# Optimization experiments

Hardware: AMD Instinct MI355X
Metric: run time of the kernel (lower is better)

The kernel has to match this reference:

```python
import jax, jax.numpy as jnp
import numpy as np

N_NODES = 50000
N_EDGES = 1200000
F_IN = 128
F_EDGE = 32
H = 78


def _p(key, shape, fan_in):
    return jax.random.normal(key, shape, dtype=jnp.float32) / np.sqrt(fan_in)


def setup_inputs() -> dict:
    key = jax.random.key(0)
    ks = jax.random.split(key, 20)
    x = jax.random.normal(ks[0], (N_NODES, F_IN), dtype=jnp.float32)
    edge_index = jax.random.randint(ks[1], (2, N_EDGES), 0, N_NODES, dtype=jnp.int32)
    edge_attr = jax.random.normal(ks[2], (N_EDGES, F_EDGE), dtype=jnp.float32)
    return {
        "x": x, "edge_index": edge_index, "edge_attr": edge_attr,
        # GATConv layer 1
        "W1": _p(ks[3], (F_IN, H), F_IN), "as1": _p(ks[4], (H,), H), "ad1": _p(ks[5], (H,), H),
        "b1": jnp.zeros((H,), jnp.float32),
        # GATConv layer 2
        "W2": _p(ks[6], (H, H), H), "as2": _p(ks[7], (H,), H), "ad2": _p(ks[8], (H,), H),
        "b2": jnp.zeros((H,), jnp.float32),
        # edge MLP
        "Wm1": _p(ks[9], (F_EDGE, H), F_EDGE), "bm1": jnp.zeros((H,), jnp.float32),
        "Wm2": _p(ks[10], (H, H), H), "bm2": jnp.zeros((H,), jnp.float32),
        # final edge head
        "Wf": _p(ks[11], (3 * H, 1), 3 * H), "bf": jnp.zeros((1,), jnp.float32),
    }


def _gat_conv(x, W, a_src, a_dst, bias, src, dst, n_nodes):
    """PyG GATConv, heads=1, negative_slope=0.2, self-loops already in src/dst."""
    h = x @ W                                   # [N, H]
    alpha_s = h @ a_src                         # [N]
    alpha_d = h @ a_dst                         # [N]
    e = jax.nn.leaky_relu(alpha_s[src] + alpha_d[dst], negative_slope=0.2)  # [E']
    # softmax over incoming edges per destination node
    m = jax.ops.segment_max(e, dst, num_segments=n_nodes)
    e = jnp.exp(e - m[dst])
    s = jax.ops.segment_sum(e, dst, num_segments=n_nodes)
    alpha = e / (s[dst] + 1e-16)                # [E']
    out = jax.ops.segment_sum(alpha[:, None] * h[src], dst, num_segments=n_nodes)
    return out + bias


def reference(x, edge_index, edge_attr, W1, as1, ad1, b1, W2, as2, ad2, b2,
              Wm1, bm1, Wm2, bm2, Wf, bf):
    n_nodes = x.shape[0]
    loop = jnp.arange(n_nodes, dtype=edge_index.dtype)
    src = jnp.concatenate([edge_index[0], loop])  # add self-loops (PyG default)
    dst = jnp.concatenate([edge_index[1], loop])

    h = _gat_conv(x, W1, as1, ad1, b1, src, dst, n_nodes)
    h = jax.nn.relu(h)  # dropout is identity in eval mode
    h = _gat_conv(h, W2, as2, ad2, b2, src, dst, n_nodes)

    ef = jax.nn.relu(edge_attr @ Wm1 + bm1) @ Wm2 + bm2            # [E, H]
    emb = jnp.concatenate([h[edge_index[0]], h[edge_index[1]], ef], axis=1)  # [E, 3H]
    return jnp.squeeze(emb @ Wf + bf, axis=-1)                     # [E]
```

## Files before the change

kernel.cpp:

```cpp
#include <hip/hip_runtime.h>
#include <math.h>

#define NN 50000
#define NE 1200000
#define FIN 128
#define FE 32
#define H 78
#define HP 80
#define ETOT (NE + NN)

#define NPB 64
#define NBUCK ((NN + NPB - 1) / NPB)
#define BCAP 2560

#define EB 3200
#define NBE ((ETOT + EB - 1) / EB)
#define GHN (NBUCK * NBE)
#define GS_NB ((GHN + 1023) / 1024)

typedef __attribute__((ext_vector_type(8))) short bf16x8;
typedef __attribute__((ext_vector_type(4))) float f32x4;

__device__ __forceinline__ unsigned short f2bf(float f) {
  unsigned u = __float_as_uint(f);
  return (unsigned short)((u + 0x7FFFu + ((u >> 16) & 1u)) >> 16);
}
__device__ __forceinline__ float bf2f(unsigned short b) {
  return __uint_as_float((unsigned)b << 16);
}

union Frag { uint4 q; bf16x8 v; unsigned short u[8]; };

__device__ __forceinline__ void wperm_one(const float* __restrict__ W, int K, int idx,
                                          uint4* __restrict__ out) {
  int lane = idx & 63;
  int fid = idx >> 6;
  int split = fid & 1;
  int sg = fid >> 1;
  int step = sg / 5, g = sg % 5;
  int kg = lane >> 4, l15 = lane & 15;
  int col = g * 16 + l15;
  Frag f;
#pragma unroll
  for (int e = 0; e < 8; ++e) {
    int k = step * 32 + kg * 8 + e;
    float v = (k < K && col < H) ? W[(size_t)k * H + col] : 0.f;
    unsigned short h = f2bf(v);
    if (split) h = f2bf(v - bf2f(h));
    f.u[e] = h;
  }
  out[idx] = f.q;
}

__global__ void prep_all(const float* __restrict__ W1, const float* __restrict__ W2,
                         const float* __restrict__ Wm2, const float* __restrict__ bm2,
                         const float* __restrict__ Wf, const float* __restrict__ bf,
                         uint4* __restrict__ wperm1, uint4* __restrict__ wperm2,
                         float* __restrict__ wpc) {
  int b = blockIdx.x, t = threadIdx.x;
  if (b < 10) {
    wperm_one(W1, FIN, b * 256 + t, wperm1);
  } else if (b < 18) {
    int idx = (b - 10) * 256 + t;
    if (idx < 30 * 64) wperm_one(W2, H, idx, wperm2);
  } else {
    int k = t;
    if (k < H) {
      float s = 0.f;
      for (int j = 0; j < H; ++j) s += Wm2[k * H + j] * Wf[2 * H + j];
      wpc[k] = s;
    } else if (k == H) {
      float s = 0.f;
      for (int j = 0; j < H; ++j) s += bm2[j] * Wf[2 * H + j];
      wpc[H] = s + bf[0];
    }
  }
}

template<int STEPS, int LDA>
__global__ __launch_bounds__(256)
void gemm_mfma(const float* __restrict__ A, const uint4* __restrict__ wperm,
               const float* __restrict__ as, const float* __restrict__ ad,
               unsigned* __restrict__ hb, float* __restrict__ asv,
               float* __restrict__ adv) {
  int lane = threadIdx.x & 63;
  int gw = blockIdx.x * 4 + (threadIdx.x >> 6);
  int n0w = gw * 16;
  if (n0w >= NN) return;
  int l15 = lane & 15, kg = lane >> 4;
  f32x4 acc[5];
#pragma unroll
  for (int g = 0; g < 5; ++g) acc[g] = (f32x4){0.f, 0.f, 0.f, 0.f};

#pragma unroll
  for (int step = 0; step < STEPS; ++step) {
    int k0 = step * 32 + kg * 8;
    bf16x8 ah, al;
    if (k0 < LDA) {
      int row = n0w + l15;
      if (row >= NN) row = NN - 1;
      const float* ar = A + (size_t)row * LDA + k0;
      float4 f0 = *reinterpret_cast<const float4*>(ar);
      float4 f1 = *reinterpret_cast<const float4*>(ar + 4);
      float fv[8] = {f0.x, f0.y, f0.z, f0.w, f1.x, f1.y, f1.z, f1.w};
#pragma unroll
      for (int e = 0; e < 8; ++e) {
        unsigned short h = f2bf(fv[e]);
        ah[e] = (short)h;
        al[e] = (short)f2bf(fv[e] - bf2f(h));
      }
    } else {
#pragma unroll
      for (int e = 0; e < 8; ++e) { ah[e] = 0; al[e] = 0; }
    }
#pragma unroll
    for (int g = 0; g < 5; ++g) {
      Frag wh, wl;
      wh.q = wperm[((size_t)(step * 5 + g) * 2 + 0) * 64 + lane];
      wl.q = wperm[((size_t)(step * 5 + g) * 2 + 1) * 64 + lane];
      acc[g] = __builtin_amdgcn_mfma_f32_16x16x32_bf16(ah, wh.v, acc[g], 0, 0, 0);
      acc[g] = __builtin_amdgcn_mfma_f32_16x16x32_bf16(al, wh.v, acc[g], 0, 0, 0);
      acc[g] = __builtin_amdgcn_mfma_f32_16x16x32_bf16(ah, wl.v, acc[g], 0, 0, 0);
    }
  }

  float asl[5], adl[5];
#pragma unroll
  for (int g = 0; g < 5; ++g) {
    int col = g * 16 + l15;
    asl[g] = (col < H) ? as[col] : 0.f;
    adl[g] = (col < H) ? ad[col] : 0.f;
  }

#pragma unroll
  for (int r = 0; r < 4; ++r) {
    int node = n0w + kg * 4 + r;
#pragma unroll
    for (int g = 0; g < 5; ++g) {
      float c = acc[g][r];
      float cn = __shfl_xor(c, 1);
      if (!(l15 & 1) && node < NN)
        hb[(size_t)node * (HP / 2) + g * 8 + (l15 >> 1)] =
            (unsigned)f2bf(c) | ((unsigned)f2bf(cn) << 16);
    }
    float sa = 0.f, sd = 0.f;
#pragma unroll
    for (int g = 0; g < 5; ++g) {
      sa = fmaf(acc[g][r], asl[g], sa);
      sd = fmaf(acc[g][r], adl[g], sd);
    }
#pragma unroll
    for (int mask = 1; mask < 16; mask <<= 1) {
      sa += __shfl_xor(sa, mask);
      sd += __shfl_xor(sd, mask);
    }
    if (l15 == 0 && node < NN) { asv[node] = sa; adv[node] = sd; }
  }
}

__global__ __launch_bounds__(256)
void bin_hist(const int* __restrict__ ei, int* __restrict__ gh) {
  __shared__ int hist[NBUCK];
  int b = blockIdx.x, t = threadIdx.x;
  for (int k = t; k < NBUCK; k += 256) hist[k] = 0;
  __syncthreads();
  int e0 = b * EB;
  int e1 = min(e0 + EB, ETOT);
  for (int i = e0 + t; i < e1; i += 256) {
    int dst = (i < NE) ? ei[NE + i] : (i - NE);
    atomicAdd(&hist[dst >> 6], 1);
  }
  __syncthreads();
  for (int k = t; k < NBUCK; k += 256) gh[(size_t)k * NBE + b] = hist[k];
}

__global__ void scan1g(const int* __restrict__ gh, int* __restrict__ gsum) {
  __shared__ int sh[256];
  int b = blockIdx.x, t = threadIdx.x;
  int i0 = b * 1024 + t * 4;
  int s = 0;
#pragma unroll
  for (int k = 0; k < 4; ++k) {
    int i = i0 + k;
    if (i < GHN) s += gh[i];
  }
  sh[t] = s;
  __syncthreads();
  for (int off = 128; off > 0; off >>= 1) {
    if (t < off) sh[t] += sh[t + off];
    __syncthreads();
  }
  if (t == 0) gsum[b] = sh[0];
}

__global__ void scan2g(const int* __restrict__ gsum, int* __restrict__ gboff) {
  __shared__ int sh[512];
  int t = threadIdx.x;
  sh[t] = (t < GS_NB) ? gsum[t] : 0;
  __syncthreads();
  for (int off = 1; off < 512; off <<= 1) {
    int v = (t >= off) ? sh[t - off] : 0;
    __syncthreads();
    sh[t] += v;
    __syncthreads();
  }
  if (t < GS_NB) gboff[t] = (t == 0) ? 0 : sh[t - 1];
}

__global__ void scan3g(const int* __restrict__ gh, const int* __restrict__ gboff,
                       int* __restrict__ goff) {
  __shared__ int sh[256];
  int b = blockIdx.x, t = threadIdx.x;
  int i0 = b * 1024 + t * 4;
  int v[4];
  int s = 0;
#pragma unroll
  for (int k = 0; k < 4; ++k) {
    int i = i0 + k;
    v[k] = (i < GHN) ? gh[i] : 0;
    s += v[k];
  }
  sh[t] = s;
  __syncthreads();
  for (int off = 1; off < 256; off <<= 1) {
    int u = (t >= off) ? sh[t - off] : 0;
    __syncthreads();
    sh[t] += u;
    __syncthreads();
  }
  int run = gboff[b] + ((t == 0) ? 0 : sh[t - 1]);
#pragma unroll
  for (int k = 0; k < 4; ++k) {
    int i = i0 + k;
    if (i < GHN) { goff[i] = run; run += v[k]; }
  }
}

__global__ __launch_bounds__(256)
void bin_place(const int* __restrict__ ei, const int* __restrict__ goff,
               unsigned long long* __restrict__ tmp) {
  __shared__ int cursor[NBUCK];
  int b = blockIdx.x, t = threadIdx.x;
  for (int k = t; k < NBUCK; k += 256) cursor[k] = goff[(size_t)k * NBE + b];
  __syncthreads();
  int e0 = b * EB;
  int e1 = min(e0 + EB, ETOT);
  for (int i = e0 + t; i < e1; i += 256) {
    int src, dst;
    if (i < NE) { src = ei[i]; dst = ei[NE + i]; }
    else { src = dst = i - NE; }
    int pos = atomicAdd(&cursor[dst >> 6], 1);
    tmp[pos] = ((unsigned long long)(unsigned)dst << 32) | (unsigned)src;
  }
}

__global__ __launch_bounds__(256)
void bucket_build(const unsigned long long* __restrict__ tmp,
                  const int* __restrict__ goff,
                  int* __restrict__ rowptr, int* __restrict__ srcs) {
  __shared__ int hist[NPB];
  __shared__ int offs[NPB];
  __shared__ int curs[NPB];
  __shared__ int srcs_l[BCAP];
  int b = blockIdx.x, t = threadIdx.x;
  int base = goff[(size_t)b * NBE];
  int next = (b + 1 < NBUCK) ? goff[(size_t)(b + 1) * NBE] : ETOT;
  int cnt = next - base;
  int n0 = b * NPB;
  if (t < NPB) hist[t] = 0;
  __syncthreads();
  for (int p = t; p < cnt; p += 256) {
    int dst = (int)(tmp[base + p] >> 32);
    atomicAdd(&hist[dst - n0], 1);
  }
  __syncthreads();
  if (t == 0) {
    int run = 0;
    for (int j = 0; j < NPB; ++j) { offs[j] = run; run += hist[j]; }
  }
  __syncthreads();
  if (t < NPB) {
    curs[t] = offs[t];
    int n = n0 + t;
    if (n < NN) rowptr[n] = base + offs[t];
  }
  if (b == NBUCK - 1 && t == 0) rowptr[NN] = ETOT;
  __syncthreads();
  for (int p = t; p < cnt; p += 256) {
    unsigned long long e = tmp[base + p];
    int dst = (int)(e >> 32);
    int src = (int)(e & 0xffffffffULL);
    int lp = atomicAdd(&curs[dst - n0], 1);
    if (lp < BCAP) srcs_l[lp] = src;
    else srcs[base + lp] = src;
  }
  __syncthreads();
  int m = cnt < BCAP ? cnt : BCAP;
  for (int p = t; p < m; p += 256) srcs[base + p] = srcs_l[p];
}

template<int RELU, int FINAL>
__global__ __launch_bounds__(256)
void gat_fused(const int* __restrict__ rowptr, const int* __restrict__ srcs,
               const float* __restrict__ asv, const float* __restrict__ adv,
               const unsigned* __restrict__ hb, const float* __restrict__ bias,
               const float* __restrict__ Wf, float* __restrict__ outp,
               float* __restrict__ uu, float* __restrict__ vv) {
  int n = (blockIdx.x * 256 + threadIdx.x) >> 6;
  int lane = threadIdx.x & 63;
  if (n >= NN) return;
  int r0 = rowptr[n], r1 = rowptr[n + 1];
  int deg = r1 - r0;
  float advn = adv[n];

  int s0 = 0;
  float e0 = -INFINITY;
  if (lane < deg) {
    s0 = srcs[r0 + lane];
    float e = asv[s0] + advn;
    e0 = e > 0.f ? e : 0.2f * e;
  }
  float m = e0;
#pragma unroll
  for (int off = 1; off < 64; off <<= 1) m = fmaxf(m, __shfl_xor(m, off));
  float ssum = (lane < deg) ? __expf(e0 - m) : 0.f;
#pragma unroll
  for (int off = 1; off < 64; off <<= 1) ssum += __shfl_xor(ssum, off);
  for (int c = r0 + 64; c < r1; c += 64) {
    int p = c + lane;
    float e = -INFINITY;
    if (p < r1) {
      float t = asv[srcs[p]] + advn;
      e = t > 0.f ? t : 0.2f * t;
    }
    float cm = e;
#pragma unroll
    for (int off = 1; off < 64; off <<= 1) cm = fmaxf(cm, __shfl_xor(cm, off));
    float c2 = (p < r1) ? __expf(e - cm) : 0.f;
#pragma unroll
    for (int off = 1; off < 64; off <<= 1) c2 += __shfl_xor(c2, off);
    float mn = fmaxf(m, cm);
    ssum = ssum * __expf(m - mn) + c2 * __expf(cm - mn);
    m = mn;
  }
  float inv = 1.f / (ssum + 1e-16f);
  float alpha0 = (lane < deg) ? __expf(e0 - m) * inv : 0.f;

  int g3 = lane / 20;
  int lp = lane - g3 * 20;
  float4 acc = {0.f, 0.f, 0.f, 0.f};
  int nch = deg < 64 ? deg : 64;
  for (int base = 0; base < nch; base += 3) {
    int p = base + g3;
    bool act = (g3 < 3) && (p < nch);
    int idx = p < 63 ? p : 63;
    float al = __shfl(alpha0, idx);
    int s = __shfl(s0, idx);
    if (act) {
      uint2 w01 = *reinterpret_cast<const uint2*>(hb + (size_t)s * (HP / 2) + lp * 2);
      acc.x = fmaf(al, bf2f((unsigned short)(w01.x & 0xffff)), acc.x);
      acc.y = fmaf(al, bf2f((unsigned short)(w01.x >> 16)), acc.y);
      acc.z = fmaf(al, bf2f((unsigned short)(w01.y & 0xffff)), acc.z);
      acc.w = fmaf(al, bf2f((unsigned short)(w01.y >> 16)), acc.w);
    }
  }
  for (int c = r0 + 64; c < r1; c += 64) {
    int p = c + lane;
    float al = 0.f;
    int s = 0;
    if (p < r1) {
      s = srcs[p];
      float t = asv[s] + advn;
      t = t > 0.f ? t : 0.2f * t;
      al = __expf(t - m) * inv;
    }
    int cnt = min(r1 - c, 64);
    for (int base = 0; base < cnt; base += 3) {
      int p2 = base + g3;
      bool act = (g3 < 3) && (p2 < cnt);
      int idx = p2 < 63 ? p2 : 63;
      float alq = __shfl(al, idx);
      int sq = __shfl(s, idx);
      if (act) {
        uint2 w01 = *reinterpret_cast<const uint2*>(hb + (size_t)sq * (HP / 2) + lp * 2);
        acc.x = fmaf(alq, bf2f((unsigned short)(w01.x & 0xffff)), acc.x);
        acc.y = fmaf(alq, bf2f((unsigned short)(w01.x >> 16)), acc.y);
        acc.z = fmaf(alq, bf2f((unsigned short)(w01.y & 0xffff)), acc.z);
        acc.w = fmaf(alq, bf2f((unsigned short)(w01.y >> 16)), acc.w);
      }
    }
  }

  float4 a1, a2;
  a1.x = __shfl(acc.x, lane + 20); a1.y = __shfl(acc.y, lane + 20);
  a1.z = __shfl(acc.z, lane + 20); a1.w = __shfl(acc.w, lane + 20);
  a2.x = __shfl(acc.x, lane + 40); a2.y = __shfl(acc.y, lane + 40);
  a2.z = __shfl(acc.z, lane + 40); a2.w = __shfl(acc.w, lane + 40);

  if (FINAL) {
    float su = 0.f, sv = 0.f;
    if (lane < 20) {
      int c0 = lane * 4;
      float o0 = acc.x + a1.x + a2.x + ((c0 + 0 < H) ? bias[c0 + 0] : 0.f);
      float o1 = acc.y + a1.y + a2.y + ((c0 + 1 < H) ? bias[c0 + 1] : 0.f);
      float o2 = acc.z + a1.z + a2.z + ((c0 + 2 < H) ? bias[c0 + 2] : 0.f);
      float o3 = acc.w + a1.w + a2.w + ((c0 + 3 < H) ? bias[c0 + 3] : 0.f);
      float wu0 = (c0 + 0 < H) ? Wf[c0 + 0] : 0.f;
      float wu1 = (c0 + 1 < H) ? Wf[c0 + 1] : 0.f;
      float wu2 = (c0 + 2 < H) ? Wf[c0 + 2] : 0.f;
      float wu3 = (c0 + 3 < H) ? Wf[c0 + 3] : 0.f;
      float wv0 = (c0 + 0 < H) ? Wf[H + c0 + 0] : 0.f;
      float wv1 = (c0 + 1 < H) ? Wf[H + c0 + 1] : 0.f;
      float wv2 = (c0 + 2 < H) ? Wf[H + c0 + 2] : 0.f;
      float wv3 = (c0 + 3 < H) ? Wf[H + c0 + 3] : 0.f;
      su = o0 * wu0 + o1 * wu1 + o2 * wu2 + o3 * wu3;
      sv = o0 * wv0 + o1 * wv1 + o2 * wv2 + o3 * wv3;
    }
#pragma unroll
    for (int off = 1; off < 64; off <<= 1) {
      su += __shfl_xor(su, off);
      sv += __shfl_xor(sv, off);
    }
    if (lane == 0) { uu[n] = su; vv[n] = sv; }
  } else {
    if (lane < 20) {
      int c0 = lane * 4;
      float4 o;
      o.x = acc.x + a1.x + a2.x + ((c0 + 0 < H) ? bias[c0 + 0] : 0.f);
      o.y = acc.y + a1.y + a2.y + ((c0 + 1 < H) ? bias[c0 + 1] : 0.f);
      o.z = acc.z + a1.z + a2.z + ((c0 + 2 < H) ? bias[c0 + 2] : 0.f);
      o.w = acc.w + a1.w + a2.w + ((c0 + 3 < H) ? bias[c0 + 3] : 0.f);
      if (RELU) {
        o.x = fmaxf(o.x, 0.f); o.y = fmaxf(o.y, 0.f);
        o.z = fmaxf(o.z, 0.f); o.w = fmaxf(o.w, 0.f);
      }
      *reinterpret_cast<float4*>(outp + (size_t)n * HP + c0) = o;
    }
  }
}

#define FE_WAVES 18750
__global__ __launch_bounds__(256)
void final_edge_mfma(const int* __restrict__ ei, const float* __restrict__ ea,
                     const float* __restrict__ Wm1, const float* __restrict__ bm1,
                     const float* __restrict__ wpc, const float* __restrict__ u,
                     const float* __restrict__ v, float* __restrict__ out) {
  int lane = threadIdx.x & 63;
  long gw = (long)blockIdx.x * 4 + (threadIdx.x >> 6);
  if (gw >= FE_WAVES) return;
  int l15 = lane & 15;
  int kg = lane >> 4;
  bf16x8 bfrag[5];
  float bm1c[5], wpcc[5];
#pragma unroll
  for (int g = 0; g < 5; ++g) {
    int col = g * 16 + l15;
    bool valid = col < H;
    bm1c[g] = valid ? bm1[col] : 0.f;
    wpcc[g] = valid ? wpc[col] : 0.f;
#pragma unroll
    for (int e = 0; e < 8; ++e) {
      int kk = kg * 8 + e;
      bfrag[g][e] = valid ? (short)f2bf(Wm1[kk * H + col]) : (short)0;
    }
  }
  float basec = wpc[H];
  int e0 = (int)(gw * 64);
#pragma unroll
  for (int t = 0; t < 4; ++t) {
    int ebase = e0 + t * 16;
    const float* ar = ea + (size_t)(ebase + l15) * FE + kg * 8;
    float4 f0 = *reinterpret_cast<const float4*>(ar);
    float4 f1 = *reinterpret_cast<const float4*>(ar + 4);
    bf16x8 afrag;
    afrag[0] = (short)f2bf(f0.x); afrag[1] = (short)f2bf(f0.y);
    afrag[2] = (short)f2bf(f0.z); afrag[3] = (short)f2bf(f0.w);
    afrag[4] = (short)f2bf(f1.x); afrag[5] = (short)f2bf(f1.y);
    afrag[6] = (short)f2bf(f1.z); afrag[7] = (short)f2bf(f1.w);
    float es0 = 0.f, es1 = 0.f, es2 = 0.f, es3 = 0.f;
#pragma unroll
    for (int g = 0; g < 5; ++g) {
      f32x4 c = {0.f, 0.f, 0.f, 0.f};
      c = __builtin_amdgcn_mfma_f32_16x16x32_bf16(afrag, bfrag[g], c, 0, 0, 0);
      es0 = fmaf(fmaxf(c[0] + bm1c[g], 0.f), wpcc[g], es0);
      es1 = fmaf(fmaxf(c[1] + bm1c[g], 0.f), wpcc[g], es1);
      es2 = fmaf(fmaxf(c[2] + bm1c[g], 0.f), wpcc[g], es2);
      es3 = fmaf(fmaxf(c[3] + bm1c[g], 0.f), wpcc[g], es3);
    }
#pragma unroll
    for (int m = 1; m < 16; m <<= 1) {
      es0 += __shfl_xor(es0, m);
      es1 += __shfl_xor(es1, m);
      es2 += __shfl_xor(es2, m);
      es3 += __shfl_xor(es3, m);
    }
    if (l15 < 4) {
      float es = (l15 == 0) ? es0 : (l15 == 1) ? es1 : (l15 == 2) ? es2 : es3;
      int e = ebase + kg * 4 + l15;
      int s = ei[e], d = ei[NE + e];
      out[e] = es + u[s] + v[d] + basec;
    }
  }
}

extern "C" void kernel_launch(void* const* d_in, const int* in_sizes, int n_in,
                              void* d_out, int out_size, void* d_ws, size_t ws_size,
                              hipStream_t stream) {
  const float* x   = (const float*)d_in[0];
  const int*   ei  = (const int*)d_in[1];
  const float* ea  = (const float*)d_in[2];
  const float* W1  = (const float*)d_in[3];
  const float* as1 = (const float*)d_in[4];
  const float* ad1 = (const float*)d_in[5];
  const float* b1  = (const float*)d_in[6];
  const float* W2  = (const float*)d_in[7];
  const float* as2 = (const float*)d_in[8];
  const float* ad2 = (const float*)d_in[9];
  const float* b2  = (const float*)d_in[10];
  const float* Wm1 = (const float*)d_in[11];
  const float* bm1 = (const float*)d_in[12];
  const float* Wm2 = (const float*)d_in[13];
  const float* bm2 = (const float*)d_in[14];
  const float* Wf  = (const float*)d_in[15];
  const float* bf  = (const float*)d_in[16];
  float* out = (float*)d_out;

  float* w = (float*)d_ws;
  float* bufB = w; w += (size_t)NN * HP;
  unsigned* hb = (unsigned*)w; w += (size_t)NN * (HP / 2);
  uint4* wperm1 = (uint4*)w; w += 4 * 40 * 64;
  uint4* wperm2 = (uint4*)w; w += 4 * 30 * 64;
  float* asv  = w; w += NN;
  float* adv  = w; w += NN;
  float* uu   = w; w += NN;
  float* vv   = w; w += NN;
  float* wpc  = w; w += HP;
  unsigned long long* tmp = (unsigned long long*)w; w += 2 * (size_t)ETOT;
  int* rowptr = (int*)w; w += NN + 1;
  int* srcs   = (int*)w; w += ETOT;
  int* gh     = (int*)w; w += GHN;
  int* goff   = (int*)w; w += GHN;
  int* gsum   = (int*)w; w += GS_NB;
  int* gboff  = (int*)w; w += GS_NB;

  const int B = 256;
  dim3 gG((NN + 63) / 64);
  dim3 gW((NN * 64 + B - 1) / B);
  dim3 gFE((FE_WAVES + 3) / 4);

  prep_all<<<19, B, 0, stream>>>(W1, W2, Wm2, bm2, Wf, bf, wperm1, wperm2, wpc);

  bin_hist<<<NBE, B, 0, stream>>>(ei, gh);
  scan1g<<<GS_NB, B, 0, stream>>>(gh, gsum);
  scan2g<<<1, 512, 0, stream>>>(gsum, gboff);
  scan3g<<<GS_NB, B, 0, stream>>>(gh, gboff, goff);
  bin_place<<<NBE, B, 0, stream>>>(ei, goff, tmp);
  bucket_build<<<NBUCK, B, 0, stream>>>(tmp, goff, rowptr, srcs);

  gemm_mfma<4, FIN><<<gG, B, 0, stream>>>(x, wperm1, as1, ad1, hb, asv, adv);
  gat_fused<1, 0><<<gW, B, 0, stream>>>(rowptr, srcs, asv, adv, hb, b1, Wf,
                                        bufB, uu, vv);

  gemm_mfma<3, HP><<<gG, B, 0, stream>>>(bufB, wperm2, as2, ad2, hb, asv, adv);
  gat_fused<0, 1><<<gW, B, 0, stream>>>(rowptr, srcs, asv, adv, hb, b2, Wf,
                                        nullptr, uu, vv);

  final_edge_mfma<<<gFE, B, 0, stream>>>(ei, ea, Wm1, bm1, wpc, uu, vv, out);
}
```

Measured before the change: 216.8 us.

## Fuse edge MLP, histogram and layer-1 GEMM into one launch; shrink sort keys

```diff
diff --git a/kernel.cpp b/kernel.cpp
--- a/kernel.cpp
+++ b/kernel.cpp
@@ -17,6 +17,10 @@
 #define NBE ((ETOT + EB - 1) / EB)
 #define GHN (NBUCK * NBE)
 #define GS_NB ((GHN + 1023) / 1024)
+
+#define GB ((NN + 63) / 64)
+#define FE_WAVES 18750
+#define FEB ((FE_WAVES + 3) / 4)
 
 typedef __attribute__((ext_vector_type(8))) short bf16x8;
 typedef __attribute__((ext_vector_type(4))) float f32x4;
@@ -78,13 +82,12 @@
 }
 
 template<int STEPS, int LDA>
-__global__ __launch_bounds__(256)
-void gemm_mfma(const float* __restrict__ A, const uint4* __restrict__ wperm,
-               const float* __restrict__ as, const float* __restrict__ ad,
-               unsigned* __restrict__ hb, float* __restrict__ asv,
-               float* __restrict__ adv) {
-  int lane = threadIdx.x & 63;
-  int gw = blockIdx.x * 4 + (threadIdx.x >> 6);
+__device__ __forceinline__ void gemm_body(const float* __restrict__ A,
+    const uint4* __restrict__ wperm, const float* __restrict__ as,
+    const float* __restrict__ ad, unsigned* __restrict__ hb,
+    float* __restrict__ asv, float* __restrict__ adv, int blk, int tid) {
+  int lane = tid & 63;
+  int gw = blk * 4 + (tid >> 6);
   int n0w = gw * 16;
   if (n0w >= NN) return;
   int l15 = lane & 15, kg = lane >> 4;
@@ -158,10 +161,9 @@
   }
 }
 
-__global__ __launch_bounds__(256)
-void bin_hist(const int* __restrict__ ei, int* __restrict__ gh) {
+__device__ __forceinline__ void bin_hist_body(const int* __restrict__ ei,
+                                              int* __restrict__ gh, int b, int t) {
   __shared__ int hist[NBUCK];
-  int b = blockIdx.x, t = threadIdx.x;
   for (int k = t; k < NBUCK; k += 256) hist[k] = 0;
   __syncthreads();
   int e0 = b * EB;
@@ -172,6 +174,89 @@
   }
   __syncthreads();
   for (int k = t; k < NBUCK; k += 256) gh[(size_t)k * NBE + b] = hist[k];
+}
+
+__device__ __forceinline__ void edge_mlp_body(const float* __restrict__ ea,
+    const float* __restrict__ Wm1, const float* __restrict__ bm1,
+    const float* __restrict__ wpc, float* __restrict__ es, int blk, int tid) {
+  int lane = tid & 63;
+  long gw = (long)blk * 4 + (tid >> 6);
+  if (gw >= FE_WAVES) return;
+  int l15 = lane & 15;
+  int kg = lane >> 4;
+  bf16x8 bfrag[5];
+  float bm1c[5], wpcc[5];
+#pragma unroll
+  for (int g = 0; g < 5; ++g) {
+    int col = g * 16 + l15;
+    bool valid = col < H;
+    bm1c[g] = valid ? bm1[col] : 0.f;
+    wpcc[g] = valid ? wpc[col] : 0.f;
+#pragma unroll
+    for (int e = 0; e < 8; ++e) {
+      int kk = kg * 8 + e;
+      bfrag[g][e] = valid ? (short)f2bf(Wm1[kk * H + col]) : (short)0;
+    }
+  }
+  float basec = wpc[H];
+  int e0 = (int)(gw * 64);
+#pragma unroll
+  for (int t4 = 0; t4 < 4; ++t4) {
+    int ebase = e0 + t4 * 16;
+    const float* ar = ea + (size_t)(ebase + l15) * FE + kg * 8;
+    float4 f0 = *reinterpret_cast<const float4*>(ar);
+    float4 f1 = *reinterpret_cast<const float4*>(ar + 4);
+    bf16x8 afrag;
+    afrag[0] = (short)f2bf(f0.x); afrag[1] = (short)f2bf(f0.y);
+    afrag[2] = (short)f2bf(f0.z); afrag[3] = (short)f2bf(f0.w);
+    afrag[4] = (short)f2bf(f1.x); afrag[5] = (short)f2bf(f1.y);
+    afrag[6] = (short)f2bf(f1.z); afrag[7] = (short)f2bf(f1.w);
+    float es0 = 0.f, es1 = 0.f, es2 = 0.f, es3 = 0.f;
+#pragma unroll
+    for (int g = 0; g < 5; ++g) {
+      f32x4 c = {0.f, 0.f, 0.f, 0.f};
+      c = __builtin_amdgcn_mfma_f32_16x16x32_bf16(afrag, bfrag[g], c, 0, 0, 0);
+      es0 = fmaf(fmaxf(c[0] + bm1c[g], 0.f), wpcc[g], es0);
+      es1 = fmaf(fmaxf(c[1] + bm1c[g], 0.f), wpcc[g], es1);
+      es2 = fmaf(fmaxf(c[2] + bm1c[g], 0.f), wpcc[g], es2);
+      es3 = fmaf(fmaxf(c[3] + bm1c[g], 0.f), wpcc[g], es3);
+    }
+#pragma unroll
+    for (int m = 1; m < 16; m <<= 1) {
+      es0 += __shfl_xor(es0, m);
+      es1 += __shfl_xor(es1, m);
+      es2 += __shfl_xor(es2, m);
+      es3 += __shfl_xor(es3, m);
+    }
+    if (l15 < 4) {
+      float esv = (l15 == 0) ? es0 : (l15 == 1) ? es1 : (l15 == 2) ? es2 : es3;
+      int e = ebase + kg * 4 + l15;
+      es[e] = esv + basec;
+    }
+  }
+}
+
+__global__ __launch_bounds__(256)
+void fuseA(const int* __restrict__ ei, int* __restrict__ gh,
+           const float* __restrict__ x, const uint4* __restrict__ wperm1,
+           const float* __restrict__ as1, const float* __restrict__ ad1,
+           unsigned* __restrict__ hb, float* __restrict__ asv,
+           float* __restrict__ adv,
+           const float* __restrict__ ea, const float* __restrict__ Wm1,
+           const float* __restrict__ bm1, const float* __restrict__ wpc,
+           float* __restrict__ es) {
+  int b = blockIdx.x, t = threadIdx.x;
+  if (b < FEB) edge_mlp_body(ea, Wm1, bm1, wpc, es, b, t);
+  else if (b < FEB + NBE) bin_hist_body(ei, gh, b - FEB, t);
+  else gemm_body<4, FIN>(x, wperm1, as1, ad1, hb, asv, adv, b - FEB - NBE, t);
+}
+
+__global__ __launch_bounds__(256)
+void gemm_mfma2(const float* __restrict__ A, const uint4* __restrict__ wperm,
+                const float* __restrict__ as, const float* __restrict__ ad,
+                unsigned* __restrict__ hb, float* __restrict__ asv,
+                float* __restrict__ adv) {
+  gemm_body<3, HP>(A, wperm, as, ad, hb, asv, adv, blockIdx.x, threadIdx.x);
 }
 
 __global__ void scan1g(const int* __restrict__ gh, int* __restrict__ gsum) {
@@ -238,7 +323,7 @@
 
 __global__ __launch_bounds__(256)
 void bin_place(const int* __restrict__ ei, const int* __restrict__ goff,
-               unsigned long long* __restrict__ tmp) {
+               unsigned* __restrict__ tmp) {
   __shared__ int cursor[NBUCK];
   int b = blockIdx.x, t = threadIdx.x;
   for (int k = t; k < NBUCK; k += 256) cursor[k] = goff[(size_t)k * NBE + b];
@@ -250,13 +335,12 @@
     if (i < NE) { src = ei[i]; dst = ei[NE + i]; }
     else { src = dst = i - NE; }
     int pos = atomicAdd(&cursor[dst >> 6], 1);
-    tmp[pos] = ((unsigned long long)(unsigned)dst << 32) | (unsigned)src;
+    tmp[pos] = ((unsigned)(dst & 63) << 17) | (unsigned)src;
   }
 }
 
 __global__ __launch_bounds__(256)
-void bucket_build(const unsigned long long* __restrict__ tmp,
-                  const int* __restrict__ goff,
+void bucket_build(const unsigned* __restrict__ tmp, const int* __restrict__ goff,
                   int* __restrict__ rowptr, int* __restrict__ srcs) {
   __shared__ int hist[NPB];
   __shared__ int offs[NPB];
@@ -270,8 +354,7 @@
   if (t < NPB) hist[t] = 0;
   __syncthreads();
   for (int p = t; p < cnt; p += 256) {
-    int dst = (int)(tmp[base + p] >> 32);
-    atomicAdd(&hist[dst - n0], 1);
+    atomicAdd(&hist[tmp[base + p] >> 17], 1);
   }
   __syncthreads();
   if (t == 0) {
@@ -287,10 +370,10 @@
   if (b == NBUCK - 1 && t == 0) rowptr[NN] = ETOT;
   __syncthreads();
   for (int p = t; p < cnt; p += 256) {
-    unsigned long long e = tmp[base + p];
-    int dst = (int)(e >> 32);
-    int src = (int)(e & 0xffffffffULL);
-    int lp = atomicAdd(&curs[dst - n0], 1);
+    unsigned e = tmp[base + p];
+    int dstoff = e >> 17;
+    int src = (int)(e & 0x1FFFFu);
+    int lp = atomicAdd(&curs[dstoff], 1);
     if (lp < BCAP) srcs_l[lp] = src;
     else srcs[base + lp] = src;
   }
@@ -346,22 +429,26 @@
   float inv = 1.f / (ssum + 1e-16f);
   float alpha0 = (lane < deg) ? __expf(e0 - m) * inv : 0.f;
 
-  int g3 = lane / 20;
-  int lp = lane - g3 * 20;
-  float4 acc = {0.f, 0.f, 0.f, 0.f};
+  int g6 = lane / 10;
+  int lp = lane - g6 * 10;
+  float4 aL = {0.f, 0.f, 0.f, 0.f}, aH = {0.f, 0.f, 0.f, 0.f};
   int nch = deg < 64 ? deg : 64;
-  for (int base = 0; base < nch; base += 3) {
-    int p = base + g3;
-    bool act = (g3 < 3) && (p < nch);
+  for (int base = 0; base < nch; base += 6) {
+    int p = base + g6;
+    bool act = (g6 < 6) && (p < nch);
     int idx = p < 63 ? p : 63;
     float al = __shfl(alpha0, idx);
     int s = __shfl(s0, idx);
     if (act) {
-      uint2 w01 = *reinterpret_cast<const uint2*>(hb + (size_t)s * (HP / 2) + lp * 2);
-      acc.x = fmaf(al, bf2f((unsigned short)(w01.x & 0xffff)), acc.x);
-      acc.y = fmaf(al, bf2f((unsigned short)(w01.x >> 16)), acc.y);
-      acc.z = fmaf(al, bf2f((unsigned short)(w01.y & 0xffff)), acc.z);
-      acc.w = fmaf(al, bf2f((unsigned short)(w01.y >> 16)), acc.w);
+      uint4 q = *(reinterpret_cast<const uint4*>(hb + (size_t)s * (HP / 2)) + lp);
+      aL.x = fmaf(al, bf2f((unsigned short)(q.x & 0xffff)), aL.x);
+      aL.y = fmaf(al, bf2f((unsigned short)(q.x >> 16)), aL.y);
+      aL.z = fmaf(al, bf2f((unsigned short)(q.y & 0xffff)), aL.z);
+      aL.w = fmaf(al, bf2f((unsigned short)(q.y >> 16)), aL.w);
+      aH.x = fmaf(al, bf2f((unsigned short)(q.z & 0xffff)), aH.x);
+      aH.y = fmaf(al, bf2f((unsigned short)(q.z >> 16)), aH.y);
+      aH.z = fmaf(al, bf2f((unsigned short)(q.w & 0xffff)), aH.z);
+      aH.w = fmaf(al, bf2f((unsigned short)(q.w >> 16)), aH.w);
     }
   }
   for (int c = r0 + 64; c < r1; c += 64) {
@@ -375,46 +462,55 @@
       al = __expf(t - m) * inv;
     }
     int cnt = min(r1 - c, 64);
-    for (int base = 0; base < cnt; base += 3) {
-      int p2 = base + g3;
-      bool act = (g3 < 3) && (p2 < cnt);
+    for (int base = 0; base < cnt; base += 6) {
+      int p2 = base + g6;
+      bool act = (g6 < 6) && (p2 < cnt);
       int idx = p2 < 63 ? p2 : 63;
       float alq = __shfl(al, idx);
       int sq = __shfl(s, idx);
       if (act) {
-        uint2 w01 = *reinterpret_cast<const uint2*>(hb + (size_t)sq * (HP / 2) + lp * 2);
-        acc.x = fmaf(alq, bf2f((unsigned short)(w01.x & 0xffff)), acc.x);
-        acc.y = fmaf(alq, bf2f((unsigned short)(w01.x >> 16)), acc.y);
-        acc.z = fmaf(alq, bf2f((unsigned short)(w01.y & 0xffff)), acc.z);
-        acc.w = fmaf(alq, bf2f((unsigned short)(w01.y >> 16)), acc.w);
+        uint4 q = *(reinterpret_cast<const uint4*>(hb + (size_t)sq * (HP / 2)) + lp);
+        aL.x = fmaf(alq, bf2f((unsigned short)(q.x & 0xffff)), aL.x);
+        aL.y = fmaf(alq, bf2f((unsigned short)(q.x >> 16)), aL.y);
+        aL.z = fmaf(alq, bf2f((unsigned short)(q.y & 0xffff)), aL.z);
+        aL.w = fmaf(alq, bf2f((unsigned short)(q.y >> 16)), aL.w);
+        aH.x = fmaf(alq, bf2f((unsigned short)(q.z & 0xffff)), aH.x);
+        aH.y = fmaf(alq, bf2f((unsigned short)(q.z >> 16)), aH.y);
+        aH.z = fmaf(alq, bf2f((unsigned short)(q.w & 0xffff)), aH.z);
+        aH.w = fmaf(alq, bf2f((unsigned short)(q.w >> 16)), aH.w);
       }
     }
   }
 
-  float4 a1, a2;
-  a1.x = __shfl(acc.x, lane + 20); a1.y = __shfl(acc.y, lane + 20);
-  a1.z = __shfl(acc.z, lane + 20); a1.w = __shfl(acc.w, lane + 20);
-  a2.x = __shfl(acc.x, lane + 40); a2.y = __shfl(acc.y, lane + 40);
-  a2.z = __shfl(acc.z, lane + 40); a2.w = __shfl(acc.w, lane + 40);
+  float o[8];
+  float* av = reinterpret_cast<float*>(&aL);
+#pragma unroll
+  for (int j = 0; j < 4; ++j) {
+    float v = av[j];
+    o[j] = v + __shfl(v, lane + 10) + __shfl(v, lane + 20) + __shfl(v, lane + 30)
+             + __shfl(v, lane + 40) + __shfl(v, lane + 50);
+  }
+  float* ah = reinterpret_cast<float*>(&aH);
+#pragma unroll
+  for (int j = 0; j < 4; ++j) {
+    float v = ah[j];
+    o[4 + j] = v + __shfl(v, lane + 10) + __shfl(v, lane + 20) + __shfl(v, lane + 30)
+                 + __shfl(v, lane + 40) + __shfl(v, lane + 50);
+  }
 
   if (FINAL) {
     float su = 0.f, sv = 0.f;
-    if (lane < 20) {
-      int c0 = lane * 4;
-      float o0 = acc.x + a1.x + a2.x + ((c0 + 0 < H) ? bias[c0 + 0] : 0.f);
-      float o1 = acc.y + a1.y + a2.y + ((c0 + 1 < H) ? bias[c0 + 1] : 0.f);
-      float o2 = acc.z + a1.z + a2.z + ((c0 + 2 < H) ? bias[c0 + 2] : 0.f);
-      float o3 = acc.w + a1.w + a2.w + ((c0 + 3 < H) ? bias[c0 + 3] : 0.f);
-      float wu0 = (c0 + 0 < H) ? Wf[c0 + 0] : 0.f;
-      float wu1 = (c0 + 1 < H) ? Wf[c0 + 1] : 0.f;
-      float wu2 = (c0 + 2 < H) ? Wf[c0 + 2] : 0.f;
-      float wu3 = (c0 + 3 < H) ? Wf[c0 + 3] : 0.f;
-      float wv0 = (c0 + 0 < H) ? Wf[H + c0 + 0] : 0.f;
-      float wv1 = (c0 + 1 < H) ? Wf[H + c0 + 1] : 0.f;
-      float wv2 = (c0 + 2 < H) ? Wf[H + c0 + 2] : 0.f;
-      float wv3 = (c0 + 3 < H) ? Wf[H + c0 + 3] : 0.f;
-      su = o0 * wu0 + o1 * wu1 + o2 * wu2 + o3 * wu3;
-      sv = o0 * wv0 + o1 * wv1 + o2 * wv2 + o3 * wv3;
+    if (lane < 10) {
+      int c0 = lane * 8;
+#pragma unroll
+      for (int j = 0; j < 8; ++j) {
+        int col = c0 + j;
+        float oj = o[j] + ((col < H) ? bias[col] : 0.f);
+        float wu = (col < H) ? Wf[col] : 0.f;
+        float wv = (col < H) ? Wf[H + col] : 0.f;
+        su = fmaf(oj, wu, su);
+        sv = fmaf(oj, wv, sv);
+      }
     }
 #pragma unroll
     for (int off = 1; off < 64; off <<= 1) {
@@ -423,84 +519,38 @@
     }
     if (lane == 0) { uu[n] = su; vv[n] = sv; }
   } else {
-    if (lane < 20) {
-      int c0 = lane * 4;
-      float4 o;
-      o.x = acc.x + a1.x + a2.x + ((c0 + 0 < H) ? bias[c0 + 0] : 0.f);
-      o.y = acc.y + a1.y + a2.y + ((c0 + 1 < H) ? bias[c0 + 1] : 0.f);
-      o.z = acc.z + a1.z + a2.z + ((c0 + 2 < H) ? bias[c0 + 2] : 0.f);
-      o.w = acc.w + a1.w + a2.w + ((c0 + 3 < H) ? bias[c0 + 3] : 0.f);
-      if (RELU) {
-        o.x = fmaxf(o.x, 0.f); o.y = fmaxf(o.y, 0.f);
-        o.z = fmaxf(o.z, 0.f); o.w = fmaxf(o.w, 0.f);
+    if (lane < 10) {
+      int c0 = lane * 8;
+      float4 w0, w1;
+      float* pw = reinterpret_cast<float*>(&w0);
+#pragma unroll
+      for (int j = 0; j < 4; ++j) {
+        int col = c0 + j;
+        float oj = o[j] + ((col < H) ? bias[col] : 0.f);
+        if (RELU) oj = fmaxf(oj, 0.f);
+        pw[j] = (col < H) ? oj : 0.f;
       }
-      *reinterpret_cast<float4*>(outp + (size_t)n * HP + c0) = o;
-    }
-  }
-}
-
-#define FE_WAVES 18750
-__global__ __launch_bounds__(256)
-void final_edge_mfma(const int* __restrict__ ei, const float* __restrict__ ea,
-                     const float* __restrict__ Wm1, const float* __restrict__ bm1,
-                     const float* __restrict__ wpc, const float* __restrict__ u,
-                     const float* __restrict__ v, float* __restrict__ out) {
-  int lane = threadIdx.x & 63;
-  long gw = (long)blockIdx.x * 4 + (threadIdx.x >> 6);
-  if (gw >= FE_WAVES) return;
-  int l15 = lane & 15;
-  int kg = lane >> 4;
-  bf16x8 bfrag[5];
-  float bm1c[5], wpcc[5];
-#pragma unroll
-  for (int g = 0; g < 5; ++g) {
-    int col = g * 16 + l15;
-    bool valid = col < H;
-    bm1c[g] = valid ? bm1[col] : 0.f;
-    wpcc[g] = valid ? wpc[col] : 0.f;
-#pragma unroll
-    for (int e = 0; e < 8; ++e) {
-      int kk = kg * 8 + e;
-      bfrag[g][e] = valid ? (short)f2bf(Wm1[kk * H + col]) : (short)0;
-    }
-  }
-  float basec = wpc[H];
-  int e0 = (int)(gw * 64);
-#pragma unroll
-  for (int t = 0; t < 4; ++t) {
-    int ebase = e0 + t * 16;
-    const float* ar = ea + (size_t)(ebase + l15) * FE + kg * 8;
-    float4 f0 = *reinterpret_cast<const float4*>(ar);
-    float4 f1 = *reinterpret_cast<const float4*>(ar + 4);
-    bf16x8 afrag;
-    afrag[0] = (short)f2bf(f0.x); afrag[1] = (short)f2bf(f0.y);
-    afrag[2] = (short)f2bf(f0.z); afrag[3] = (short)f2bf(f0.w);
-    afrag[4] = (short)f2bf(f1.x); afrag[5] = (short)f2bf(f1.y);
-    afrag[6] = (short)f2bf(f1.z); afrag[7] = (short)f2bf(f1.w);
-    float es0 = 0.f, es1 = 0.f, es2 = 0.f, es3 = 0.f;
-#pragma unroll
-    for (int g = 0; g < 5; ++g) {
-      f32x4 c = {0.f, 0.f, 0.f, 0.f};
-      c = __builtin_amdgcn_mfma_f32_16x16x32_bf16(afrag, bfrag[g], c, 0, 0, 0);
-      es0 = fmaf(fmaxf(c[0] + bm1c[g], 0.f), wpcc[g], es0);
-      es1 = fmaf(fmaxf(c[1] + bm1c[g], 0.f), wpcc[g], es1);
-      es2 = fmaf(fmaxf(c[2] + bm1c[g], 0.f), wpcc[g], es2);
-      es3 = fmaf(fmaxf(c[3] + bm1c[g], 0.f), wpcc[g], es3);
-    }
-#pragma unroll
-    for (int m = 1; m < 16; m <<= 1) {
-      es0 += __shfl_xor(es0, m);
-      es1 += __shfl_xor(es1, m);
-      es2 += __shfl_xor(es2, m);
-      es3 += __shfl_xor(es3, m);
-    }
-    if (l15 < 4) {
-      float es = (l15 == 0) ? es0 : (l15 == 1) ? es1 : (l15 == 2) ? es2 : es3;
-      int e = ebase + kg * 4 + l15;
-      int s = ei[e], d = ei[NE + e];
-      out[e] = es + u[s] + v[d] + basec;
-    }
-  }
+      float* pw1 = reinterpret_cast<float*>(&w1);
+#pragma unroll
+      for (int j = 0; j < 4; ++j) {
+        int col = c0 + 4 + j;
+        float oj = o[4 + j] + ((col < H) ? bias[col] : 0.f);
+        if (RELU) oj = fmaxf(oj, 0.f);
+        pw1[j] = (col < H) ? oj : 0.f;
+      }
+      float* orow = outp + (size_t)n * HP + c0;
+      *reinterpret_cast<float4*>(orow) = w0;
+      *reinterpret_cast<float4*>(orow + 4) = w1;
+    }
+  }
+}
+
+__global__ void final_out(const float* __restrict__ es, const int* __restrict__ ei,
+                          const float* __restrict__ u, const float* __restrict__ v,
+                          float* __restrict__ out) {
+  int e = blockIdx.x * blockDim.x + threadIdx.x;
+  if (e >= NE) return;
+  out[e] = es[e] + u[ei[e]] + v[ei[NE + e]];
 }
 
 extern "C" void kernel_launch(void* const* d_in, const int* in_sizes, int n_in,
@@ -535,7 +585,8 @@
   float* uu   = w; w += NN;
   float* vv   = w; w += NN;
   float* wpc  = w; w += HP;
-  unsigned long long* tmp = (unsigned long long*)w; w += 2 * (size_t)ETOT;
+  float* es   = w; w += NE;
+  unsigned* tmp = (unsigned*)w; w += ETOT;
   int* rowptr = (int*)w; w += NN + 1;
   int* srcs   = (int*)w; w += ETOT;
   int* gh     = (int*)w; w += GHN;
@@ -544,26 +595,26 @@
   int* gboff  = (int*)w; w += GS_NB;
 
   const int B = 256;
-  dim3 gG((NN + 63) / 64);
   dim3 gW((NN * 64 + B - 1) / B);
-  dim3 gFE((FE_WAVES + 3) / 4);
+  dim3 gEo((NE + B - 1) / B);
 
   prep_all<<<19, B, 0, stream>>>(W1, W2, Wm2, bm2, Wf, bf, wperm1, wperm2, wpc);
 
-  bin_hist<<<NBE, B, 0, stream>>>(ei, gh);
+  fuseA<<<FEB + NBE + GB, B, 0, stream>>>(ei, gh, x, wperm1, as1, ad1, hb, asv,
+                                          adv, ea, Wm1, bm1, wpc, es);
+
   scan1g<<<GS_NB, B, 0, stream>>>(gh, gsum);
   scan2g<<<1, 512, 0, stream>>>(gsum, gboff);
   scan3g<<<GS_NB, B, 0, stream>>>(gh, gboff, goff);
   bin_place<<<NBE, B, 0, stream>>>(ei, goff, tmp);
   bucket_build<<<NBUCK, B, 0, stream>>>(tmp, goff, rowptr, srcs);
 
-  gemm_mfma<4, FIN><<<gG, B, 0, stream>>>(x, wperm1, as1, ad1, hb, asv, adv);
   gat_fused<1, 0><<<gW, B, 0, stream>>>(rowptr, srcs, asv, adv, hb, b1, Wf,
                                         bufB, uu, vv);
 
-  gemm_mfma<3, HP><<<gG, B, 0, stream>>>(bufB, wperm2, as2, ad2, hb, asv, adv);
+  gemm_mfma2<<<GB, B, 0, stream>>>(bufB, wperm2, as2, ad2, hb, asv, adv);
   gat_fused<0, 1><<<gW, B, 0, stream>>>(rowptr, srcs, asv, adv, hb, b2, Wf,
                                         nullptr, uu, vv);
 
-  final_edge_mfma<<<gFE, B, 0, stream>>>(ei, ea, Wm1, bm1, wpc, uu, vv, out);
-}
+  final_out<<<gEo, B, 0, stream>>>(es, ei, uu, vv, out);
+}
```

New measurement: 221.4 us. 1.02x slower.
